# Performance work log

Hardware: AMD Instinct MI355X
Metric: run time of the kernel (lower is better)

Reference implementation:

```python
import jax, jax.numpy as jnp
import numpy as np

N_NODES = 50000
N_EDGES = 1600000
NFEAT = 512
NHID = 64
H1 = 8      # nheads[0]
H2 = 1      # nheads[1]
NCLASS = 16
ALPHA = 0.2  # leaky_relu negative slope


def setup_inputs() -> dict:
    key = jax.random.key(0)
    ks = jax.random.split(key, 6)
    x = jax.random.normal(ks[0], (N_NODES, NFEAT), jnp.float32)
    edge_index = jax.random.randint(ks[1], (2, N_EDGES), 0, N_NODES, jnp.int32)

    def glorot(k, shape):
        fan_in, fan_out = shape[-2], shape[-1]
        std = (2.0 / (fan_in + fan_out)) ** 0.5
        return jax.random.normal(k, shape, jnp.float32) * std

    W1 = glorot(ks[2], (H1, NFEAT, NHID))
    a1 = jax.random.normal(ks[3], (H1, 2 * NHID), jnp.float32) * 0.1
    W2 = glorot(ks[4], (H2, NHID * H1, NCLASS))
    a2 = jax.random.normal(ks[5], (H2, 2 * NCLASS), jnp.float32) * 0.1
    return {"x": x, "edge_index": edge_index, "W1": W1, "a1": a1, "W2": W2, "a2": a2}


def _spgat_head(x, W, a, src, dst, n_nodes, apply_elu):
    # Sparse GAT head (pyGAT SpGraphAttentionLayer, eval mode / no dropout).
    h = x @ W                              # [N, F']
    f = W.shape[1]
    # a . [h_src || h_dst] decomposed into per-node scores (same math, no [E,2F'] concat)
    s_src = h @ a[:f]                      # [N]
    s_dst = h @ a[f:]                      # [N]
    logits = s_src[src] + s_dst[dst]       # [E]
    e = jnp.exp(-jax.nn.leaky_relu(logits, ALPHA))  # edge_e = exp(-leakyrelu(...)) > 0
    rowsum = jax.ops.segment_sum(e, src, num_segments=n_nodes)            # [N]
    agg = jax.ops.segment_sum(e[:, None] * h[dst], src, num_segments=n_nodes)  # [N, F']
    h_prime = agg / rowsum[:, None]
    return jax.nn.elu(h_prime) if apply_elu else h_prime


def reference(x, edge_index, W1, a1, W2, a2):
    src, dst = edge_index[0], edge_index[1]
    n = x.shape[0]
    # Layer 1: H1 heads, concat=True (elu inside each head), concatenated on features
    h = jnp.concatenate(
        [_spgat_head(x, W1[i], a1[i], src, dst, n, True) for i in range(W1.shape[0])],
        axis=1,
    )  # [N, H1*NHID]
    # Layer 2: H2 heads, concat=False, stacked then averaged
    outs = jnp.stack(
        [_spgat_head(h, W2[i], a2[i], src, dst, n, False) for i in range(W2.shape[0])],
        axis=2,
    )  # [N, NCLASS, H2]
    out = jnp.mean(outs, axis=2)
    return jax.nn.log_softmax(jax.nn.elu(out), axis=1)
```

## Files before the change

### kernel.cpp

```cpp
#include <hip/hip_runtime.h>

#define NN 50000
#define NE 1600000
#define NFEAT 512
#define NHID 64
#define H1 8
#define NCLASS 16
#define ALPHA 0.2f

#define BUCKETS 391
#define CAP 6144
#define EPB 4096
#define PASSA_BLKS 391
#define PASSB_BLKS 391
#define PACK_BLKS 1024
#define PACK2_BLKS 32
#define GEMMB 391
#define NROW_PAD 50048

typedef __attribute__((ext_vector_type(8))) short short8;
typedef __attribute__((ext_vector_type(4))) float floatx4;
typedef __attribute__((ext_vector_type(2))) float floatx2;
typedef __attribute__((ext_vector_type(2))) long longx2;

__device__ __forceinline__ float elu_f(float x) { return x > 0.0f ? x : __expf(x) - 1.0f; }
__device__ __forceinline__ float edge_w(float logit) {
    return __expf(-fmaxf(logit, ALPHA * logit));
}
__device__ __forceinline__ ushort f2bf(float f) {
    uint u = __float_as_uint(f);
    return (ushort)((u + 0x7FFFu + ((u >> 16) & 1)) >> 16);
}
__device__ __forceinline__ uint packbf2(float lo, float hi) {
    return (uint)f2bf(lo) | ((uint)f2bf(hi) << 16);
}
__device__ __forceinline__ float bf2f(ushort v) { return __uint_as_float((uint)v << 16); }
__device__ __forceinline__ unsigned char f2fp8(float v) {
    return (unsigned char)(__builtin_amdgcn_cvt_pk_fp8_f32(v, v, 0, false) & 0xFF);
}
__device__ __forceinline__ uint pack4fp8(float a, float b, float c, float d) {
    uint u = __builtin_amdgcn_cvt_pk_fp8_f32(a, b, 0, false);
    return __builtin_amdgcn_cvt_pk_fp8_f32(c, d, u, true);
}

#define GLD16(g, l)                                                              \
    __builtin_amdgcn_global_load_lds(                                            \
        (const __attribute__((address_space(1))) unsigned int*)(g),              \
        (__attribute__((address_space(3))) unsigned int*)(l), 16, 0, 0)

__device__ __forceinline__ int scan256x(int v, int tid, int* wsum, int* tot) {
    int s = v;
#pragma unroll
    for (int o = 1; o < 64; o <<= 1) {
        int u = __shfl_up(s, o);
        if ((tid & 63) >= o) s += u;
    }
    __syncthreads();
    if ((tid & 63) == 63) wsum[tid >> 6] = s;
    __syncthreads();
    int off = 0, t = 0;
#pragma unroll
    for (int i = 0; i < 4; i++) {
        int x = wsum[i];
        if (i < (tid >> 6)) off += x;
        t += x;
    }
    *tot = t;
    return s - v + off;
}

__device__ __forceinline__ int scan512x(int v, int tid, int* wsum, int* tot) {
    int s = v;
#pragma unroll
    for (int o = 1; o < 64; o <<= 1) {
        int u = __shfl_up(s, o);
        if ((tid & 63) >= o) s += u;
    }
    __syncthreads();
    if ((tid & 63) == 63) wsum[tid >> 6] = s;
    __syncthreads();
    int off = 0, t = 0;
#pragma unroll
    for (int i = 0; i < 8; i++) {
        int x = wsum[i];
        if (i < (tid >> 6)) off += x;
        t += x;
    }
    *tot = t;
    return s - v + off;
}

__global__ __launch_bounds__(256) void prep_k(const float* __restrict__ W1,
                                              unsigned char* __restrict__ Wt8,
                                              const float* __restrict__ W2,
                                              ushort* __restrict__ W2tb,
                                              const int* __restrict__ ei,
                                              int* __restrict__ bucket_cnt,
                                              uint* __restrict__ staging) {
    int b = blockIdx.x;
    if (b < PACK_BLKS) {
        int i = b * 256 + threadIdx.x;
        int c = i >> 9, o = i & 511;
        int c6 = o >> 6, qhi = (o >> 4) & 3, kb = (o >> 3) & 1, bb = o & 7;
        int quad = qhi ^ ((c >> 1) & 3);
        int k = c6 * 64 + kb * 32 + quad * 8 + bb;
        Wt8[i] = f2fp8(W1[((c >> 6) * 512 + k) * 64 + (c & 63)]);
        return;
    }
    if (b < PACK_BLKS + PACK2_BLKS) {
        int i = (b - PACK_BLKS) * 256 + threadIdx.x;
        int c = i >> 9, f = i & 511;
        W2tb[i] = f2bf(W2[f * 16 + c]);
        return;
    }
    __shared__ int histA[BUCKETS];
    __shared__ int exclA[BUCKETS];
    __shared__ int baseA[BUCKETS];
    __shared__ int wsumA[4];
    __shared__ uint ebuf[EPB];
    const int blk = b - PACK_BLKS - PACK2_BLKS;
    const int t = threadIdx.x;
    const int e0 = blk * EPB;
    const int cntb = min(EPB, NE - e0);
    for (int i = t; i < BUCKETS; i += 256) histA[i] = 0;
    __syncthreads();
    int br[16]; uint pay[16];
#pragma unroll
    for (int i = 0; i < 16; i++) {
        int e = e0 + i * 256 + t;
        br[i] = -1;
        if (e < NE) {
            int s = ei[e], d = ei[NE + e];
            int bu = s >> 7;
            pay[i] = ((uint)bu << 23) | ((uint)(s & 127) << 16) | (uint)d;
            br[i] = (bu << 12) | atomicAdd(&histA[bu], 1);
        }
    }
    __syncthreads();
    int tot0, tot1;
    int v0 = histA[t];
    int v1 = (t + 256 < BUCKETS) ? histA[t + 256] : 0;
    int p0 = scan256x(v0, t, wsumA, &tot0);
    int p1 = scan256x(v1, t, wsumA, &tot1);
    exclA[t] = p0;
    if (t + 256 < BUCKETS) exclA[t + 256] = p1 + tot0;
    __syncthreads();
    for (int i = t; i < BUCKETS; i += 256) {
        int c = histA[i];
        if (c > 0) baseA[i] = atomicAdd(&bucket_cnt[i], c);
    }
#pragma unroll
    for (int i = 0; i < 16; i++)
        if (br[i] >= 0) ebuf[exclA[br[i] >> 12] + (br[i] & 4095)] = pay[i];
    __syncthreads();
    for (int j = t; j < cntb; j += 256) {
        uint v = ebuf[j];
        int bu = v >> 23;
        int pos = baseA[bu] + (j - exclA[bu]);
        staging[(size_t)bu * CAP + pos] = v;
    }
}

__global__ __launch_bounds__(512) void passb_gemm1_k(const int* __restrict__ bucket_cnt,
                                                     const uint* __restrict__ staging,
                                                     ushort* __restrict__ csru,
                                                     int* __restrict__ rowptr,
                                                     const float* __restrict__ x,
                                                     const unsigned char* __restrict__ Wt8,
                                                     const float* __restrict__ a1,
                                                     unsigned char* __restrict__ h8,
                                                     float* __restrict__ s1s,
                                                     float* __restrict__ s1d) {
    __shared__ unsigned char shmem[32768];
    const int tid = threadIdx.x;

    if (blockIdx.x < PASSB_BLKS) {
        int* hist2 = (int*)shmem;
        int* excl2 = hist2 + 128;
        int* cur2 = excl2 + 128;
        int* wsum2 = cur2 + 128;
        __shared__ int sbs;
        const int b = blockIdx.x;
        const int cnt = bucket_cnt[b];
        const uint* sg = staging + (size_t)b * CAP;
        if (tid < 128) { hist2[tid] = 0; cur2[tid] = 0; }
        if (tid < 64) {
            int c[7]; int s0 = 0;
#pragma unroll
            for (int i = 0; i < 7; i++) {
                int bi = tid * 7 + i;
                c[i] = (bi < BUCKETS) ? bucket_cnt[bi] : 0;
                s0 += c[i];
            }
            int sc = s0;
#pragma unroll
            for (int o = 1; o < 64; o <<= 1) {
                int u = __shfl_up(sc, o);
                if (tid >= o) sc += u;
            }
            int run = sc - s0;
            if (tid == b / 7) {
                int part = run;
                for (int i = 0; i < b % 7; i++) part += c[i];
                sbs = part;
            }
        }
        if (b == 0 && tid == 0) rowptr[NN] = NE;
        __syncthreads();
        const int sbase = sbs;
        for (int e = tid; e < cnt; e += 512) atomicAdd(&hist2[(sg[e] >> 16) & 127], 1);
        __syncthreads();
        int v = (tid < 128) ? hist2[tid] : 0;
        int tot;
        int ex = scan512x(v, tid, wsum2, &tot);
        if (tid < 128) {
            excl2[tid] = ex;
            int n = b * 128 + tid;
            if (n < NN) rowptr[n] = sbase + ex;
        }
        __syncthreads();
        for (int e = tid; e < cnt; e += 512) {
            uint u = sg[e];
            int sl = (u >> 16) & 127;
            int pos = excl2[sl] + atomicAdd(&cur2[sl], 1);
            csru[sbase + pos] = (ushort)(u & 0xFFFF);
        }
        return;
    }

    unsigned char* Bs = shmem;
    const int gb = blockIdx.x - PASSB_BLKS;
    const int row0 = gb * 128;
    const int wv = tid >> 6, lane = tid & 63;
    const int l16 = lane & 15, quad = lane >> 4;
    const int qoff = ((quad ^ ((l16 >> 1) & 3)) << 4);
    const int mA = wv * 16 + (lane >> 2);
    const int offA = (lane & 3) * 16;
    const unsigned char* gB0 = Wt8 + (size_t)(0 * 128 + mA) * 512 + offA;
    const unsigned char* gB1 = Wt8 + (size_t)(1 * 128 + mA) * 512 + offA;
    const unsigned char* gB2 = Wt8 + (size_t)(2 * 128 + mA) * 512 + offA;
    const unsigned char* gB3 = Wt8 + (size_t)(3 * 128 + mA) * 512 + offA;
    const int arow = row0 + wv * 16 + l16;
    const float* xA = x + (size_t)arow * 512 + quad * 8;

    floatx4 acc[32];
#pragma unroll
    for (int ct = 0; ct < 32; ct++) acc[ct] = (floatx4){0.f, 0.f, 0.f, 0.f};

    for (int t = 0; t < 8; t++) {
        const int k0 = t * 64;
        GLD16(gB0 + k0, Bs + wv * 1024);
        GLD16(gB1 + k0, Bs + 8192 + wv * 1024);
        GLD16(gB2 + k0, Bs + 16384 + wv * 1024);
        GLD16(gB3 + k0, Bs + 24576 + wv * 1024);
        float4 f0 = *(const float4*)(xA + k0);
        float4 f1 = *(const float4*)(xA + k0 + 4);
        float4 f2 = *(const float4*)(xA + k0 + 32);
        float4 f3 = *(const float4*)(xA + k0 + 36);
        uint u0 = pack4fp8(f0.x, f0.y, f0.z, f0.w);
        uint u1 = pack4fp8(f1.x, f1.y, f1.z, f1.w);
        uint u2 = pack4fp8(f2.x, f2.y, f2.z, f2.w);
        uint u3 = pack4fp8(f3.x, f3.y, f3.z, f3.w);
        long ax = (long)(((unsigned long)u1 << 32) | u0);
        long ay = (long)(((unsigned long)u3 << 32) | u2);
        __syncthreads();
        const unsigned char* bp = Bs + l16 * 64 + qoff;
#pragma unroll
        for (int ct = 0; ct < 32; ct++) {
            longx2 bv = *(const longx2*)(bp + ct * 1024);
            acc[ct] = __builtin_amdgcn_mfma_f32_16x16x32_fp8_fp8(ax, bv.x, acc[ct], 0, 0, 0);
            acc[ct] = __builtin_amdgcn_mfma_f32_16x16x32_fp8_fp8(ay, bv.y, acc[ct], 0, 0, 0);
        }
        __syncthreads();
    }

    const int rbase = row0 + wv * 16 + quad * 4;
#pragma unroll
    for (int hh = 0; hh < 8; hh++) {
        float ss[4] = {0.f, 0.f, 0.f, 0.f}, sd[4] = {0.f, 0.f, 0.f, 0.f};
#pragma unroll
        for (int c4 = 0; c4 < 4; c4++) {
            int ct = hh * 4 + c4;
            int colg = ct * 16 + l16;
            float avs = a1[hh * 128 + c4 * 16 + l16];
            float avd = a1[hh * 128 + 64 + c4 * 16 + l16];
#pragma unroll
            for (int r = 0; r < 4; r++) {
                float v = acc[ct][r];
                ss[r] += v * avs;
                sd[r] += v * avd;
                int row = rbase + r;
                if (row < NN) h8[(size_t)row * 512 + colg] = f2fp8(v);
            }
        }
#pragma unroll
        for (int r = 0; r < 4; r++) {
            float a_ = ss[r], b_ = sd[r];
#pragma unroll
            for (int o = 1; o < 16; o <<= 1) {
                a_ += __shfl_xor(a_, o);
                b_ += __shfl_xor(b_, o);
            }
            int row = rbase + r;
            if (l16 == 0 && row < NN) {
                s1s[row * 8 + hh] = a_;
                s1d[row * 8 + hh] = b_;
            }
        }
    }
}

__global__ __launch_bounds__(256) void agg1f_k(const int* __restrict__ rowptr,
                                               const ushort* __restrict__ csru,
                                               const float* __restrict__ s1s,
                                               const float* __restrict__ s1d,
                                               const uint2* __restrict__ hb8,
                                               const ushort* __restrict__ W2tb,
                                               const float* __restrict__ a2,
                                               ushort* __restrict__ h2b,
                                               float* __restrict__ s2s,
                                               float* __restrict__ s2d) {
    __shared__ ushort Ash[16 * 512];
    unsigned char* ashb = (unsigned char*)Ash;
    const int tid = threadIdx.x;
    const int wv = tid >> 6, lane = tid & 63;
    const int n0 = blockIdx.x * 4;
    const int n = n0 + wv;
    const int head8 = lane >> 3;
    const int hb = head8 << 3;
    const int esub = lane & 7;
    const int beg = rowptr[n];
    const int deg = rowptr[n + 1] - beg;
    const float ssrc = s1s[n * 8 + head8];
    floatx2 acc[4] = {};
    float rsum = 0.f;

    const int G = (deg + 7) >> 3;
    const int dm1 = deg - 1;
    if (G > 0) {
        int dA = csru[beg + min(esub, dm1)];
        float tw = s1d[dA * 8 + head8];
        for (int g = 0; g < G; g++) {
            uint2 v[8];
#pragma unroll
            for (int j = 0; j < 8; j++) {
                int dj = __shfl(dA, j);
                v[j] = hb8[(uint)dj * 64 + lane];
            }
            int dAn = csru[beg + min(g * 8 + 8 + esub, dm1)];
            float twn = s1d[dAn * 8 + head8];
            float w = (g * 8 + esub <= dm1) ? edge_w(ssrc + tw) : 0.f;
            rsum += w;
#pragma unroll
            for (int j = 0; j < 8; j++) {
                float wj = __shfl(w, hb + j);
                floatx2 w2 = (floatx2){wj, wj};
                acc[0] += w2 * __builtin_amdgcn_cvt_pk_f32_fp8(v[j].x, false);
                acc[1] += w2 * __builtin_amdgcn_cvt_pk_f32_fp8(v[j].x, true);
                acc[2] += w2 * __builtin_amdgcn_cvt_pk_f32_fp8(v[j].y, false);
                acc[3] += w2 * __builtin_amdgcn_cvt_pk_f32_fp8(v[j].y, true);
            }
            dA = dAn;
            tw = twn;
        }
    }

    rsum += __shfl_xor(rsum, 1);
    rsum += __shfl_xor(rsum, 2);
    rsum += __shfl_xor(rsum, 4);
    float inv = 1.0f / rsum;
    uint4 o;
    o.x = packbf2(elu_f(acc[0][0] * inv), elu_f(acc[0][1] * inv));
    o.y = packbf2(elu_f(acc[1][0] * inv), elu_f(acc[1][1] * inv));
    o.z = packbf2(elu_f(acc[2][0] * inv), elu_f(acc[2][1] * inv));
    o.w = packbf2(elu_f(acc[3][0] * inv), elu_f(acc[3][1] * inv));
    *(uint4*)(ashb + wv * 1024 + ((lane * 16) ^ (wv << 4))) = o;
    __syncthreads();

    if (wv == 0) {
        const int l16 = lane & 15, q = lane >> 4;
        floatx4 c2 = (floatx4){0.f, 0.f, 0.f, 0.f};
#pragma unroll
        for (int s = 0; s < 16; s++) {
            short8 af = *(const short8*)(ashb + l16 * 1024 +
                                         ((s * 64 + q * 16) ^ ((l16 & 7) << 4)));
            short8 bf = *(const short8*)(W2tb + l16 * 512 + s * 32 + q * 8);
            c2 = __builtin_amdgcn_mfma_f32_16x16x32_bf16(af, bf, c2, 0, 0, 0);
        }
        if (q == 0) {
#pragma unroll
            for (int r = 0; r < 4; r++) h2b[(size_t)(n0 + r) * 16 + l16] = f2bf(c2[r]);
        }
#pragma unroll
        for (int r = 0; r < 4; r++) {
            float ssv = c2[r] * a2[l16];
            float sdv = c2[r] * a2[16 + l16];
#pragma unroll
            for (int oo = 1; oo < 16; oo <<= 1) {
                ssv += __shfl_xor(ssv, oo);
                sdv += __shfl_xor(sdv, oo);
            }
            if (lane == 0) { s2s[n0 + r] = ssv; s2d[n0 + r] = sdv; }
        }
    }
}

__global__ __launch_bounds__(256) void agg2_k(const int* __restrict__ rowptr,
                                              const ushort* __restrict__ csru,
                                              const float* __restrict__ s2s,
                                              const float* __restrict__ s2d,
                                              const ushort* __restrict__ h2b,
                                              float* __restrict__ out) {
    const int n = (blockIdx.x * 256 + threadIdx.x) >> 6;
    const int lane = threadIdx.x & 63;
    if (n >= NN) return;
    const int beg = rowptr[n], end = rowptr[n + 1];
    const float sn = s2s[n];
    const int sub = lane >> 4, f = lane & 15;
    float acc = 0.f, rsum = 0.f;
    int e = beg + sub;
    for (; e + 12 < end; e += 16) {
        int d0 = csru[e], d1 = csru[e + 4], d2 = csru[e + 8], d3 = csru[e + 12];
        float t0 = s2d[d0], t1 = s2d[d1], t2 = s2d[d2], t3 = s2d[d3];
        float g0 = bf2f(h2b[(uint)d0 * 16 + f]), g1 = bf2f(h2b[(uint)d1 * 16 + f]);
        float g2 = bf2f(h2b[(uint)d2 * 16 + f]), g3 = bf2f(h2b[(uint)d3 * 16 + f]);
        float w0 = edge_w(sn + t0), w1 = edge_w(sn + t1);
        float w2 = edge_w(sn + t2), w3 = edge_w(sn + t3);
        acc += w0 * g0 + w1 * g1 + w2 * g2 + w3 * g3;
        rsum += w0 + w1 + w2 + w3;
    }
    for (; e < end; e += 4) {
        int d0 = csru[e];
        float w0 = edge_w(sn + s2d[d0]);
        acc += w0 * bf2f(h2b[(uint)d0 * 16 + f]);
        rsum += w0;
    }
    acc += __shfl_down(acc, 32);
    acc += __shfl_down(acc, 16);
    rsum += __shfl_down(rsum, 32);
    rsum += __shfl_down(rsum, 16);
    if (lane < 16) {
        float v = elu_f(acc / rsum);
        float m = v;
#pragma unroll
        for (int o = 8; o > 0; o >>= 1) m = fmaxf(m, __shfl_xor(m, o));
        float ex = __expf(v - m), s = ex;
#pragma unroll
        for (int o = 8; o > 0; o >>= 1) s += __shfl_xor(s, o);
        out[(size_t)n * 16 + f] = v - (__logf(s) + m);
    }
}

extern "C" void kernel_launch(void* const* d_in, const int* in_sizes, int n_in,
                              void* d_out, int out_size, void* d_ws, size_t ws_size,
                              hipStream_t stream) {
    const float* x  = (const float*)d_in[0];
    const int*   ei = (const int*)d_in[1];
    const float* W1 = (const float*)d_in[2];
    const float* a1 = (const float*)d_in[3];
    const float* W2 = (const float*)d_in[4];
    const float* a2 = (const float*)d_in[5];
    float* out = (float*)d_out;

    unsigned char* h8  = (unsigned char*)d_ws;
    unsigned char* Wt8 = h8 + (size_t)NROW_PAD * 512;
    ushort* W2tb  = (ushort*)(Wt8 + 512 * 512);
    float* s1s    = (float*)(W2tb + 8192);
    float* s1d    = s1s + (size_t)NN * H1;
    int* rowptr   = (int*)(s1d + (size_t)NN * H1);
    int* bucket_cnt   = rowptr + 50056;
    int* bucket_start = bucket_cnt + 512;
    ushort* csru  = (ushort*)(bucket_start + 512);
    ushort* h2b   = csru + NE;
    float* s2s    = (float*)(h2b + (size_t)NN * 16);
    float* s2d    = s2s + NN;
    uint* staging = (uint*)(s2d + NN);

    hipMemsetAsync(bucket_cnt, 0, 512 * sizeof(int), stream);

    prep_k<<<PACK_BLKS + PACK2_BLKS + PASSA_BLKS, 256, 0, stream>>>(
        W1, Wt8, W2, W2tb, ei, bucket_cnt, staging);
    passb_gemm1_k<<<PASSB_BLKS + GEMMB, 512, 0, stream>>>(bucket_cnt, staging, csru, rowptr,
                                                          x, Wt8, a1, h8, s1s, s1d);
    agg1f_k<<<NN / 4, 256, 0, stream>>>(rowptr, csru, s1s, s1d,
                                        (const uint2*)h8, W2tb, a2, h2b, s2s, s2d);
    agg2_k<<<(NN + 3) / 4, 256, 0, stream>>>(rowptr, csru, s2s, s2d, h2b, out);
}
```

Baseline: 391.5 us.

## Split fused GEMM1 into 64-row by 256-column tiles with 256-thread blocks

```diff
diff --git a/kernel.cpp b/kernel.cpp
--- a/kernel.cpp
+++ b/kernel.cpp
@@ -15,7 +15,8 @@
 #define PASSB_BLKS 391
 #define PACK_BLKS 1024
 #define PACK2_BLKS 32
-#define GEMMB 391
+#define ROWB 782
+#define GEMM_BLKS (2 * ROWB)
 #define NROW_PAD 50048
 
 typedef __attribute__((ext_vector_type(8))) short short8;
@@ -61,27 +62,6 @@
     int off = 0, t = 0;
 #pragma unroll
     for (int i = 0; i < 4; i++) {
-        int x = wsum[i];
-        if (i < (tid >> 6)) off += x;
-        t += x;
-    }
-    *tot = t;
-    return s - v + off;
-}
-
-__device__ __forceinline__ int scan512x(int v, int tid, int* wsum, int* tot) {
-    int s = v;
-#pragma unroll
-    for (int o = 1; o < 64; o <<= 1) {
-        int u = __shfl_up(s, o);
-        if ((tid & 63) >= o) s += u;
-    }
-    __syncthreads();
-    if ((tid & 63) == 63) wsum[tid >> 6] = s;
-    __syncthreads();
-    int off = 0, t = 0;
-#pragma unroll
-    for (int i = 0; i < 8; i++) {
         int x = wsum[i];
         if (i < (tid >> 6)) off += x;
         t += x;
@@ -161,7 +141,7 @@
     }
 }
 
-__global__ __launch_bounds__(512) void passb_gemm1_k(const int* __restrict__ bucket_cnt,
+__global__ __launch_bounds__(256) void passb_gemm1_k(const int* __restrict__ bucket_cnt,
                                                      const uint* __restrict__ staging,
                                                      ushort* __restrict__ csru,
                                                      int* __restrict__ rowptr,
@@ -171,7 +151,7 @@
                                                      unsigned char* __restrict__ h8,
                                                      float* __restrict__ s1s,
                                                      float* __restrict__ s1d) {
-    __shared__ unsigned char shmem[32768];
+    __shared__ unsigned char shmem[16384];
     const int tid = threadIdx.x;
 
     if (blockIdx.x < PASSB_BLKS) {
@@ -208,18 +188,18 @@
         if (b == 0 && tid == 0) rowptr[NN] = NE;
         __syncthreads();
         const int sbase = sbs;
-        for (int e = tid; e < cnt; e += 512) atomicAdd(&hist2[(sg[e] >> 16) & 127], 1);
+        for (int e = tid; e < cnt; e += 256) atomicAdd(&hist2[(sg[e] >> 16) & 127], 1);
         __syncthreads();
         int v = (tid < 128) ? hist2[tid] : 0;
         int tot;
-        int ex = scan512x(v, tid, wsum2, &tot);
+        int ex = scan256x(v, tid, wsum2, &tot);
         if (tid < 128) {
             excl2[tid] = ex;
             int n = b * 128 + tid;
             if (n < NN) rowptr[n] = sbase + ex;
         }
         __syncthreads();
-        for (int e = tid; e < cnt; e += 512) {
+        for (int e = tid; e < cnt; e += 256) {
             uint u = sg[e];
             int sl = (u >> 16) & 127;
             int pos = excl2[sl] + atomicAdd(&cur2[sl], 1);
@@ -230,29 +210,27 @@
 
     unsigned char* Bs = shmem;
     const int gb = blockIdx.x - PASSB_BLKS;
-    const int row0 = gb * 128;
+    const int rb = gb >> 1, ch = gb & 1;
+    const int row0 = rb * 64;
+    const int colbase = ch * 256;
     const int wv = tid >> 6, lane = tid & 63;
     const int l16 = lane & 15, quad = lane >> 4;
     const int qoff = ((quad ^ ((l16 >> 1) & 3)) << 4);
-    const int mA = wv * 16 + (lane >> 2);
-    const int offA = (lane & 3) * 16;
-    const unsigned char* gB0 = Wt8 + (size_t)(0 * 128 + mA) * 512 + offA;
-    const unsigned char* gB1 = Wt8 + (size_t)(1 * 128 + mA) * 512 + offA;
-    const unsigned char* gB2 = Wt8 + (size_t)(2 * 128 + mA) * 512 + offA;
-    const unsigned char* gB3 = Wt8 + (size_t)(3 * 128 + mA) * 512 + offA;
+    const unsigned char* gBt = Wt8 + (size_t)(colbase + (tid >> 2)) * 512 + (tid & 3) * 16;
     const int arow = row0 + wv * 16 + l16;
-    const float* xA = x + (size_t)arow * 512 + quad * 8;
-
-    floatx4 acc[32];
-#pragma unroll
-    for (int ct = 0; ct < 32; ct++) acc[ct] = (floatx4){0.f, 0.f, 0.f, 0.f};
+    const int arowc = min(arow, NN - 1);
+    const float* xA = x + (size_t)arowc * 512 + quad * 8;
+
+    floatx4 acc[16];
+#pragma unroll
+    for (int ct = 0; ct < 16; ct++) acc[ct] = (floatx4){0.f, 0.f, 0.f, 0.f};
 
     for (int t = 0; t < 8; t++) {
         const int k0 = t * 64;
-        GLD16(gB0 + k0, Bs + wv * 1024);
-        GLD16(gB1 + k0, Bs + 8192 + wv * 1024);
-        GLD16(gB2 + k0, Bs + 16384 + wv * 1024);
-        GLD16(gB3 + k0, Bs + 24576 + wv * 1024);
+        GLD16(gBt + k0, Bs + tid * 16);
+        GLD16(gBt + k0 + 32768, Bs + 4096 + tid * 16);
+        GLD16(gBt + k0 + 65536, Bs + 8192 + tid * 16);
+        GLD16(gBt + k0 + 98304, Bs + 12288 + tid * 16);
         float4 f0 = *(const float4*)(xA + k0);
         float4 f1 = *(const float4*)(xA + k0 + 4);
         float4 f2 = *(const float4*)(xA + k0 + 32);
@@ -266,7 +244,7 @@
         __syncthreads();
         const unsigned char* bp = Bs + l16 * 64 + qoff;
 #pragma unroll
-        for (int ct = 0; ct < 32; ct++) {
+        for (int ct = 0; ct < 16; ct++) {
             longx2 bv = *(const longx2*)(bp + ct * 1024);
             acc[ct] = __builtin_amdgcn_mfma_f32_16x16x32_fp8_fp8(ax, bv.x, acc[ct], 0, 0, 0);
             acc[ct] = __builtin_amdgcn_mfma_f32_16x16x32_fp8_fp8(ay, bv.y, acc[ct], 0, 0, 0);
@@ -276,14 +254,15 @@
 
     const int rbase = row0 + wv * 16 + quad * 4;
 #pragma unroll
-    for (int hh = 0; hh < 8; hh++) {
+    for (int hh = 0; hh < 4; hh++) {
+        const int head = (colbase >> 6) + hh;
         float ss[4] = {0.f, 0.f, 0.f, 0.f}, sd[4] = {0.f, 0.f, 0.f, 0.f};
 #pragma unroll
         for (int c4 = 0; c4 < 4; c4++) {
             int ct = hh * 4 + c4;
-            int colg = ct * 16 + l16;
-            float avs = a1[hh * 128 + c4 * 16 + l16];
-            float avd = a1[hh * 128 + 64 + c4 * 16 + l16];
+            int colg = colbase + ct * 16 + l16;
+            float avs = a1[head * 128 + c4 * 16 + l16];
+            float avd = a1[head * 128 + 64 + c4 * 16 + l16];
 #pragma unroll
             for (int r = 0; r < 4; r++) {
                 float v = acc[ct][r];
@@ -303,8 +282,8 @@
             }
             int row = rbase + r;
             if (l16 == 0 && row < NN) {
-                s1s[row * 8 + hh] = a_;
-                s1d[row * 8 + hh] = b_;
+                s1s[row * 8 + head] = a_;
+                s1d[row * 8 + head] = b_;
             }
         }
     }
@@ -480,8 +459,9 @@
 
     prep_k<<<PACK_BLKS + PACK2_BLKS + PASSA_BLKS, 256, 0, stream>>>(
         W1, Wt8, W2, W2tb, ei, bucket_cnt, staging);
-    passb_gemm1_k<<<PASSB_BLKS + GEMMB, 512, 0, stream>>>(bucket_cnt, staging, csru, rowptr,
-                                                          x, Wt8, a1, h8, s1s, s1d);
+    passb_gemm1_k<<<PASSB_BLKS + GEMM_BLKS, 256, 0, stream>>>(bucket_cnt, staging, csru,
+                                                              rowptr, x, Wt8, a1, h8,
+                                                              s1s, s1d);
     agg1f_k<<<NN / 4, 256, 0, stream>>>(rowptr, csru, s1s, s1d,
                                         (const uint2*)h8, W2tb, a2, h2b, s2s, s2d);
     agg2_k<<<(NN + 3) / 4, 256, 0, stream>>>(rowptr, csru, s2s, s2d, h2b, out);
```

After: 395.2 us. Within noise of the previous version (+0.9%).
